# Kernel optimization log

Hardware: AMD Instinct MI355X
Metric: run time of the kernel (lower is better)

## Reference

```python
import jax, jax.numpy as jnp
import numpy as np

IMPOSSIBLE = -10000.0
K = 5  # BIOUL tag states per label: O, I, B, L, U


def _bioul_transitions():
    O, I, B, L, U = 0, 1, 2, 3, 4
    allowed = np.zeros((K, K), dtype=bool)
    for f, ts in {O: [O, B, U], B: [I, L], I: [I, L], L: [O, B, U], U: [O, B, U]}.items():
        allowed[f, ts] = True
    trans = jnp.asarray(np.where(allowed, 0.0, IMPOSSIBLE), dtype=jnp.float32)
    start = jnp.asarray([0.0, IMPOSSIBLE, 0.0, IMPOSSIBLE, 0.0], dtype=jnp.float32)  # O,B,U may start
    end = jnp.asarray([0.0, IMPOSSIBLE, IMPOSSIBLE, 0.0, 0.0], dtype=jnp.float32)    # O,L,U may end
    return trans, start, end


def _crf_marginal(emissions, mask):
    # Linear-chain CRF forward-backward log-marginals.
    # emissions: [N, T, K] float, mask: [N, T] bool (contiguous right-padded).
    trans, start, end = _bioul_transitions()
    e = jnp.swapaxes(emissions, 0, 1)   # [T, N, K]
    m = jnp.swapaxes(mask, 0, 1)        # [T, N]
    N = e.shape[1]

    alpha0 = start[None, :] + e[0]

    def fwd_step(alpha, xs):
        et, mt = xs
        new = jax.nn.logsumexp(alpha[:, :, None] + trans[None, :, :], axis=1) + et
        alpha = jnp.where(mt[:, None], new, alpha)  # carry alpha through padding
        return alpha, alpha

    alpha_last, alphas_rest = jax.lax.scan(fwd_step, alpha0, (e[1:], m[1:]))
    alphas = jnp.concatenate([alpha0[None], alphas_rest], axis=0)  # [T, N, K]
    logZ = jax.nn.logsumexp(alpha_last + end[None, :], axis=-1)    # [N]

    # Backward pass: beta_t excludes emission at t; beta at last valid token = end.
    m_next = jnp.concatenate([m[1:], jnp.zeros((1, N), dtype=bool)], axis=0)
    e_next = jnp.concatenate([e[1:], jnp.zeros_like(e[:1])], axis=0)

    def bwd_step(beta, xs):
        en, mt, mn = xs  # emis_{t+1}, mask_t, mask_{t+1}
        cand = jax.nn.logsumexp(trans[None, :, :] + (en + beta)[:, None, :], axis=2)
        beta = jnp.where((mt & ~mn)[:, None], end[None, :], cand)
        return beta, beta

    _, betas_rev = jax.lax.scan(
        bwd_step,
        jnp.broadcast_to(end, (N, K)),
        (e_next[::-1], m[::-1], m_next[::-1]),
    )
    betas = betas_rev[::-1]  # [T, N, K]

    logm = alphas + betas - logZ[None, :, None]
    return jnp.swapaxes(logm, 0, 1)  # [N, T, K]


def _forward(embeds, W, b, mask, tags):
    N, T, D = embeds.shape
    n_labels = tags.shape[1]
    logits = jnp.einsum('ntd,kd->ntk', embeds, W) + b  # [N, T, n_labels*K]
    crf_logits = logits.reshape(N, T, n_labels, K).transpose(0, 2, 1, 3).reshape(N * n_labels, T, K)
    crf_mask = jnp.repeat(mask, n_labels, axis=0)       # [N*n_labels, T] (repeat_interleave on dim 0)
    target = (tags[..., None] == jnp.arange(K)).reshape(N * n_labels, T, K)  # bool one-hot
    logm = _crf_marginal(crf_logits, crf_mask)
    lse = jax.nn.logsumexp(
        jnp.where(target, jax.nn.log_softmax(logm, axis=-1), IMPOSSIBLE), axis=-1
    )
    loss = -jnp.where(crf_mask, lse, 0.0).sum()
    return loss / 100.0


def setup_inputs() -> dict:
    key = jax.random.key(0)
    kE, kW, kb, kT, kL = jax.random.split(key, 5)
    N, T, D, n_labels = 64, 1024, 512, 24
    embeds = jax.random.normal(kE, (N, T, D), dtype=jnp.float32)
    W = jax.random.normal(kW, (n_labels * K, D), dtype=jnp.float32) * 0.02
    b = jax.random.normal(kb, (n_labels * K,), dtype=jnp.float32) * 0.02
    tags = jax.random.randint(kT, (N, n_labels, T), 0, K, dtype=jnp.int32)
    lengths = jax.random.randint(kL, (N,), T // 2, T + 1)
    mask = jnp.arange(T)[None, :] < lengths[:, None]  # right-padded variable lengths
    return {"embeds": embeds, "W": W, "b": b, "mask": mask, "tags": tags}


def reference(embeds, W, b, mask, tags):
    return _forward(embeds, W, b, mask, tags)
```

## Files before the change

### kernel.cpp

```cpp
#include <hip/hip_runtime.h>
#include <hip/hip_bf16.h>

#define IMP -10000.0f

#define O_BH   0u
#define O_BL   131072u
#define O_LEN  262144u
#define O_ACC  262400u
#define O_TT   262656u
#define O_E    6554112u
#define O_P    38011392u
#define O_Q    41157120u
#define O_FS   44302848u
#define O_BS   45875712u

typedef __attribute__((ext_vector_type(8))) short bf16x8;
typedef __attribute__((ext_vector_type(4))) float f32x4;

__device__ __forceinline__ float lse2(float a, float b) {
    float m = fmaxf(a, b);
    return m + __logf(__expf(a - m) + __expf(b - m));
}

__device__ __forceinline__ unsigned short f2bf(float x) {
    unsigned u = __float_as_uint(x);
    return (unsigned short)((u + 0x7FFFu + ((u >> 16) & 1u)) >> 16);
}
__device__ __forceinline__ float bf2f(unsigned short h) {
    return __uint_as_float(((unsigned)h) << 16);
}

__global__ __launch_bounds__(256) void prep_kernel(const unsigned char* __restrict__ mask,
                                                   int* __restrict__ lens,
                                                   double* __restrict__ acc) {
    int n = blockIdx.x;
    int tid = threadIdx.x;
    bool i32 = (mask[1] == 0);
    int cnt = 0;
    if (i32) {
        const int* m = (const int*)mask;
        for (int t = tid; t < 1024; t += 256) cnt += (m[n * 1024 + t] != 0);
    } else {
        for (int t = tid; t < 1024; t += 256) cnt += (mask[n * 1024 + t] != 0);
    }
    __shared__ int red[256];
    red[tid] = cnt;
    __syncthreads();
    for (int s = 128; s > 0; s >>= 1) {
        if (tid < s) red[tid] += red[tid + s];
        __syncthreads();
    }
    if (tid == 0) {
        lens[n] = red[0];
        if (n == 0) *acc = 0.0;
    }
}

__global__ __launch_bounds__(256) void tagsT_kernel(const int* __restrict__ tags,
                                                    int* __restrict__ tagsT) {
    int idx = blockIdx.x * 256 + threadIdx.x;
    int t = idx / 1536, s = idx - t * 1536;
    tagsT[idx] = tags[(size_t)s * 1024 + t];
}

__global__ __launch_bounds__(256) void prepW_kernel(const float* __restrict__ W,
                                                    short* __restrict__ Bh,
                                                    short* __restrict__ Bl) {
    int idx = blockIdx.x * 256 + threadIdx.x;
    int col = idx >> 9, k = idx & 511;
    float v = (col < 120) ? W[col * 512 + k] : 0.f;
    unsigned short h = f2bf(v);
    unsigned short l = f2bf(v - bf2f(h));
    int ct = col >> 4, c = col & 15;
    int kt = k >> 5, kg = (k >> 3) & 3, i = k & 7;
    size_t flat = ((size_t)(kt * 8 + ct) * 64 + kg * 16 + c) * 8 + i;
    Bh[flat] = (short)h;
    Bl[flat] = (short)l;
}

__global__ __launch_bounds__(256) void mfma_gemm(const float* __restrict__ A,
                                                 const short* __restrict__ Bh,
                                                 const short* __restrict__ Bl,
                                                 const float* __restrict__ bias,
                                                 float* __restrict__ E) {
    __shared__ short Ah[4][128][8];
    __shared__ short Al[4][128][8];
    int tid = threadIdx.x;
    int wave = tid >> 6, lane = tid & 63;
    long r0 = (long)blockIdx.x * 128;

    f32x4 acc[8][2];
#pragma unroll
    for (int rt = 0; rt < 8; ++rt)
#pragma unroll
        for (int ci = 0; ci < 2; ++ci) {
            acc[rt][ci][0] = 0.f; acc[rt][ci][1] = 0.f;
            acc[rt][ci][2] = 0.f; acc[rt][ci][3] = 0.f;
        }

    float bb[2];
#pragma unroll
    for (int ci = 0; ci < 2; ++ci) {
        int col = wave * 32 + ci * 16 + (lane & 15);
        bb[ci] = (col < 120) ? bias[col] : 0.f;
    }

    int arow = lane & 15;
    int akg = lane >> 4;

    for (int kt = 0; kt < 16; ++kt) {
        __syncthreads();
#pragma unroll
        for (int i = 0; i < 4; ++i) {
            int f = tid + (i << 8);
            int row = f >> 3, fq = f & 7;
            const float4 v = *(const float4*)(A + (r0 + row) * 512 + kt * 32 + fq * 4);
            int kgw = fq >> 1, i0 = (fq & 1) * 4;
            unsigned short h0 = f2bf(v.x), h1 = f2bf(v.y), h2 = f2bf(v.z), h3 = f2bf(v.w);
            short4 hv = make_short4((short)h0, (short)h1, (short)h2, (short)h3);
            short4 lv = make_short4((short)f2bf(v.x - bf2f(h0)), (short)f2bf(v.y - bf2f(h1)),
                                    (short)f2bf(v.z - bf2f(h2)), (short)f2bf(v.w - bf2f(h3)));
            *(short4*)&Ah[kgw][row][i0] = hv;
            *(short4*)&Al[kgw][row][i0] = lv;
        }
        __syncthreads();

        bf16x8 bh[2], bl[2];
#pragma unroll
        for (int ci = 0; ci < 2; ++ci) {
            int ct = wave * 2 + ci;
            size_t base = ((size_t)(kt * 8 + ct) * 64 + lane) * 8;
            bh[ci] = *(const bf16x8*)(Bh + base);
            bl[ci] = *(const bf16x8*)(Bl + base);
        }

#pragma unroll
        for (int rt = 0; rt < 8; ++rt) {
            bf16x8 ah = *(const bf16x8*)&Ah[akg][rt * 16 + arow][0];
            bf16x8 al = *(const bf16x8*)&Al[akg][rt * 16 + arow][0];
#pragma unroll
            for (int ci = 0; ci < 2; ++ci) {
                acc[rt][ci] = __builtin_amdgcn_mfma_f32_16x16x32_bf16(ah, bh[ci], acc[rt][ci], 0, 0, 0);
                acc[rt][ci] = __builtin_amdgcn_mfma_f32_16x16x32_bf16(ah, bl[ci], acc[rt][ci], 0, 0, 0);
                acc[rt][ci] = __builtin_amdgcn_mfma_f32_16x16x32_bf16(al, bh[ci], acc[rt][ci], 0, 0, 0);
            }
        }
    }

#pragma unroll
    for (int rt = 0; rt < 8; ++rt) {
#pragma unroll
        for (int ci = 0; ci < 2; ++ci) {
            int col = wave * 32 + ci * 16 + (lane & 15);
            if (col < 120) {
#pragma unroll
                for (int j = 0; j < 4; ++j) {
                    long r = r0 + rt * 16 + (lane >> 4) * 4 + j;
                    int n = (int)(r >> 10), t = (int)(r & 1023);
                    E[(size_t)t * 7680 + n * 120 + col] = acc[rt][ci][j] + bb[ci];
                }
            }
        }
    }
}

__global__ __launch_bounds__(256) void chunkops_kernel(const float* __restrict__ E,
                                                       const int* __restrict__ lens,
                                                       float* __restrict__ P,
                                                       float* __restrict__ Q,
                                                       float* __restrict__ BS) {
    int s = blockIdx.x * 256 + threadIdx.x;
    int c = blockIdx.y;
    int t0 = c << 3;
    int len = lens[s / 24];
    const float* ep = E + (size_t)t0 * 7680 + s * 5;
    bool fullQ = (t0 + 8 <= len - 1);

    float e[9][5];
#pragma unroll
    for (int j = 0; j < 8; ++j) {
        const float* q = ep + (size_t)j * 7680;
        e[j][0] = q[0]; e[j][1] = q[1]; e[j][2] = q[2]; e[j][3] = q[3]; e[j][4] = q[4];
    }
    if (fullQ) {
        const float* q = ep + (size_t)8 * 7680;
        e[8][0] = q[0]; e[8][1] = q[1]; e[8][2] = q[2]; e[8][3] = q[3]; e[8][4] = q[4];
    }

    {
        float r00 = lse2(e[0][0], e[0][4]), r01 = e[0][3], r10 = e[0][2], r11 = e[0][1];
#pragma unroll
        for (int j = 1; j < 8; ++j) {
            float m00 = lse2(e[j][0], e[j][4]), m01 = e[j][3], m10 = e[j][2], m11 = e[j][1];
            float n00 = lse2(m00 + r00, m01 + r10);
            float n01 = lse2(m00 + r01, m01 + r11);
            float n10 = lse2(m10 + r00, m11 + r10);
            float n11 = lse2(m10 + r01, m11 + r11);
            r00 = n00; r01 = n01; r10 = n10; r11 = n11;
        }
        float4 v; v.x = r00; v.y = r01; v.z = r10; v.w = r11;
        *(float4*)(P + ((size_t)c * 1536 + s) * 4) = v;
    }

    if (fullQ) {
        float r00 = lse2(e[1][0], e[1][4]), r01 = e[1][2], r10 = e[1][3], r11 = e[1][1];
#pragma unroll
        for (int j = 1; j < 8; ++j) {
            float g0 = e[j + 1][0], g1 = e[j + 1][1], g2 = e[j + 1][2], g3 = e[j + 1][3],
                  g4 = e[j + 1][4];
            float n00 = lse2(g0, g4), n01 = g2, n10 = g3, n11 = g1;
            float m00 = lse2(r00 + n00, r01 + n10);
            float m01 = lse2(r00 + n01, r01 + n11);
            float m10 = lse2(r10 + n00, r11 + n10);
            float m11 = lse2(r10 + n01, r11 + n11);
            r00 = m00; r01 = m01; r10 = m10; r11 = m11;
        }
        float4 v; v.x = r00; v.y = r01; v.z = r10; v.w = r11;
        *(float4*)(Q + ((size_t)c * 1536 + s) * 4) = v;
    } else if (t0 <= len - 1) {
        float X = 0.f, Y = IMP;
#pragma unroll
        for (int j = 6; j >= 0; --j) {
            if (t0 + j <= len - 2) {
                float g0 = e[j + 1][0], g1 = e[j + 1][1], g2 = e[j + 1][2], g3 = e[j + 1][3],
                      g4 = e[j + 1][4];
                float nX = lse2(lse2(g0, g4) + X, g2 + Y);
                float nY = lse2(g3 + X, g1 + Y);
                X = nX; Y = nY;
            }
        }
        float2 v; v.x = X; v.y = Y;
        *(float2*)(BS + ((size_t)c * 1536 + s) * 2) = v;
    }
}

__global__ __launch_bounds__(64) void combine_kernel(const float* __restrict__ P,
                                                     const float* __restrict__ Q,
                                                     const int* __restrict__ lens,
                                                     float* __restrict__ FS,
                                                     float* __restrict__ BS) {
    int s = blockIdx.x * 64 + threadIdx.x;
    float x = 0.f, y = IMP;
    for (int c = 0; c < 128; ++c) {
        float2 v; v.x = x; v.y = y;
        *(float2*)(FS + ((size_t)c * 1536 + s) * 2) = v;
        float4 p = *(const float4*)(P + ((size_t)c * 1536 + s) * 4);
        float nx = lse2(p.x + x, p.y + y);
        float ny = lse2(p.z + x, p.w + y);
        x = nx; y = ny;
    }
    int len = lens[s / 24];
    int cb = (len - 1) >> 3;
    float2 b = *(const float2*)(BS + ((size_t)cb * 1536 + s) * 2);
    float X = b.x, Y = b.y;
    for (int c = cb - 1; c >= 0; --c) {
        float4 q = *(const float4*)(Q + ((size_t)c * 1536 + s) * 4);
        float nX = lse2(q.x + X, q.y + Y);
        float nY = lse2(q.z + X, q.w + Y);
        X = nX; Y = nY;
        float2 v; v.x = X; v.y = Y;
        *(float2*)(BS + ((size_t)c * 1536 + s) * 2) = v;
    }
}

__global__ __launch_bounds__(256) void loss_kernel(const float* __restrict__ E,
                                                   const int* __restrict__ lens,
                                                   const float* __restrict__ FS,
                                                   const float* __restrict__ BS,
                                                   const int* __restrict__ tagsT,
                                                   double* __restrict__ acc) {
    int s = blockIdx.x * 256 + threadIdx.x;
    int c = blockIdx.y;
    int t0 = c << 3;
    int len = lens[s / 24];
    double Lv = 0.0;

    if (t0 < len) {
        int cb = (len - 1) >> 3;
        int nt = min(8, len - t0);
        const float* ep = E + (size_t)t0 * 7680 + s * 5;

        float ev[8][5];
#pragma unroll
        for (int j = 0; j < 8; ++j) {
            if (j < nt) {
                const float* q = ep + (size_t)j * 7680;
                ev[j][0] = q[0]; ev[j][1] = q[1]; ev[j][2] = q[2]; ev[j][3] = q[3]; ev[j][4] = q[4];
            }
        }
        float e8[5] = {0.f, 0.f, 0.f, 0.f, 0.f};
        if (c < cb) {
            const float* q = ep + (size_t)8 * 7680;
            e8[0] = q[0]; e8[1] = q[1]; e8[2] = q[2]; e8[3] = q[3]; e8[4] = q[4];
        }
        int tg[8];
#pragma unroll
        for (int j = 0; j < 8; ++j) tg[j] = tagsT[(size_t)(t0 + j) * 1536 + s];

        float2 f = *(const float2*)(FS + ((size_t)c * 1536 + s) * 2);
        float x = f.x, y = f.y;
        float xs[8], ys[8];
#pragma unroll
        for (int j = 0; j < 8; ++j) {
            if (j < nt) {
                xs[j] = x; ys[j] = y;
                float nx = lse2(lse2(ev[j][0], ev[j][4]) + x, ev[j][3] + y);
                float ny = lse2(ev[j][2] + x, ev[j][1] + y);
                x = nx; y = ny;
            }
        }

        float X = 0.f, Y = IMP;
        if (c < cb) {
            float2 bb = *(const float2*)(BS + ((size_t)(c + 1) * 1536 + s) * 2);
            X = bb.x; Y = bb.y;
        }
#pragma unroll
        for (int j = 7; j >= 0; --j) {
            if (j >= nt) continue;
            if (c == cb && j == nt - 1) {
                X = 0.f; Y = IMP;
            } else {
                float g0, g1, g2, g3, g4;
                if (j == 7) { g0 = e8[0]; g1 = e8[1]; g2 = e8[2]; g3 = e8[3]; g4 = e8[4]; }
                else { g0 = ev[j + 1][0]; g1 = ev[j + 1][1]; g2 = ev[j + 1][2];
                       g3 = ev[j + 1][3]; g4 = ev[j + 1][4]; }
                float nX = lse2(lse2(g0, g4) + X, g2 + Y);
                float nY = lse2(g3 + X, g1 + Y);
                X = nX; Y = nY;
            }
            float v0 = xs[j] + ev[j][0] + X, v1 = ys[j] + ev[j][1] + Y, v2 = xs[j] + ev[j][2] + Y;
            float v3 = ys[j] + ev[j][3] + X, v4 = xs[j] + ev[j][4] + X;
            int tag = tg[j];
            float m = fmaxf(fmaxf(fmaxf(fmaxf(v0, v1), v2), v3), v4);
            float ssum = __expf(v0 - m) + __expf(v1 - m) + __expf(v2 - m) +
                         __expf(v3 - m) + __expf(v4 - m);
            float lse = m + __logf(ssum);
            float vt = (tag == 0) ? v0 : (tag == 1) ? v1 : (tag == 2) ? v2 : (tag == 3) ? v3 : v4;
            float ls = vt - lse;
            float mm = fmaxf(ls, IMP);
            float term = mm + __logf(__expf(ls - mm) + 4.0f * __expf(IMP - mm));
            Lv += (double)term;
        }
    }

    __shared__ double red[256];
    red[threadIdx.x] = Lv;
    __syncthreads();
    for (int st = 128; st > 0; st >>= 1) {
        if (threadIdx.x < st) red[threadIdx.x] += red[threadIdx.x + st];
        __syncthreads();
    }
    if (threadIdx.x == 0) atomicAdd(acc, red[0]);
}

__global__ void finalize_kernel(const double* __restrict__ acc, float* __restrict__ out) {
    out[0] = (float)(-(*acc) * 0.01);
}

extern "C" void kernel_launch(void* const* d_in, const int* in_sizes, int n_in,
                              void* d_out, int out_size, void* d_ws, size_t ws_size,
                              hipStream_t stream) {
    const float* embeds = (const float*)d_in[0];
    const float* W = (const float*)d_in[1];
    const float* bias = (const float*)d_in[2];
    const unsigned char* mask = (const unsigned char*)d_in[3];
    const int* tags = (const int*)d_in[4];
    float* out = (float*)d_out;

    char* ws = (char*)d_ws;
    short* Bh = (short*)(ws + O_BH);
    short* Bl = (short*)(ws + O_BL);
    int* lens = (int*)(ws + O_LEN);
    double* acc = (double*)(ws + O_ACC);
    int* tagsT = (int*)(ws + O_TT);
    float* E = (float*)(ws + O_E);
    float* P = (float*)(ws + O_P);
    float* Q = (float*)(ws + O_Q);
    float* FS = (float*)(ws + O_FS);
    float* BS = (float*)(ws + O_BS);

    prep_kernel<<<64, 256, 0, stream>>>(mask, lens, acc);
    prepW_kernel<<<256, 256, 0, stream>>>(W, Bh, Bl);
    tagsT_kernel<<<6144, 256, 0, stream>>>(tags, tagsT);
    mfma_gemm<<<512, 256, 0, stream>>>(embeds, Bh, Bl, bias, E);
    chunkops_kernel<<<dim3(6, 128), 256, 0, stream>>>(E, lens, P, Q, BS);
    combine_kernel<<<24, 64, 0, stream>>>(P, Q, lens, FS, BS);
    loss_kernel<<<dim3(6, 128), 256, 0, stream>>>(E, lens, FS, BS, tagsT, acc);
    finalize_kernel<<<1, 1, 0, stream>>>(acc, out);
}
```

Before: 329.9 us.

## Replace serial chunk combine with parallel log-semiring prefix scan

New measurement: 273.8 us. 17.0% less time.

```diff
diff --git a/kernel.cpp b/kernel.cpp
--- a/kernel.cpp
+++ b/kernel.cpp
@@ -20,6 +20,15 @@
 __device__ __forceinline__ float lse2(float a, float b) {
     float m = fmaxf(a, b);
     return m + __logf(__expf(a - m) + __expf(b - m));
+}
+
+__device__ __forceinline__ float4 matmul22(float4 A, float4 B) {
+    float4 r;
+    r.x = lse2(A.x + B.x, A.y + B.z);
+    r.y = lse2(A.x + B.y, A.y + B.w);
+    r.z = lse2(A.z + B.x, A.w + B.z);
+    r.w = lse2(A.z + B.y, A.w + B.w);
+    return r;
 }
 
 __device__ __forceinline__ unsigned short f2bf(float x) {
@@ -234,32 +243,64 @@
     }
 }
 
-__global__ __launch_bounds__(64) void combine_kernel(const float* __restrict__ P,
-                                                     const float* __restrict__ Q,
-                                                     const int* __restrict__ lens,
-                                                     float* __restrict__ FS,
-                                                     float* __restrict__ BS) {
-    int s = blockIdx.x * 64 + threadIdx.x;
-    float x = 0.f, y = IMP;
-    for (int c = 0; c < 128; ++c) {
-        float2 v; v.x = x; v.y = y;
-        *(float2*)(FS + ((size_t)c * 1536 + s) * 2) = v;
-        float4 p = *(const float4*)(P + ((size_t)c * 1536 + s) * 4);
-        float nx = lse2(p.x + x, p.y + y);
-        float ny = lse2(p.z + x, p.w + y);
-        x = nx; y = ny;
-    }
+__global__ __launch_bounds__(128) void combine_kernel(const float* __restrict__ P,
+                                                      const float* __restrict__ Q,
+                                                      const int* __restrict__ lens,
+                                                      float* __restrict__ FS,
+                                                      float* __restrict__ BS) {
+    int s = blockIdx.x;
+    int c = threadIdx.x;
+    __shared__ float4 ops[128];
+
+    float4 v = *(const float4*)(P + ((size_t)c * 1536 + s) * 4);
+    ops[c] = v;
+    __syncthreads();
+#pragma unroll
+    for (int d = 1; d < 128; d <<= 1) {
+        float4 other;
+        bool act = (c >= d);
+        if (act) other = ops[c - d];
+        __syncthreads();
+        if (act) { v = matmul22(v, other); ops[c] = v; }
+        __syncthreads();
+    }
+    float2 fs;
+    if (c == 0) {
+        fs.x = 0.f; fs.y = IMP;
+    } else {
+        float4 m = ops[c - 1];
+        fs.x = lse2(m.x, m.y + IMP);
+        fs.y = lse2(m.z, m.w + IMP);
+    }
+    *(float2*)(FS + ((size_t)c * 1536 + s) * 2) = fs;
+
     int len = lens[s / 24];
     int cb = (len - 1) >> 3;
     float2 b = *(const float2*)(BS + ((size_t)cb * 1536 + s) * 2);
-    float X = b.x, Y = b.y;
-    for (int c = cb - 1; c >= 0; --c) {
-        float4 q = *(const float4*)(Q + ((size_t)c * 1536 + s) * 4);
-        float nX = lse2(q.x + X, q.y + Y);
-        float nY = lse2(q.z + X, q.w + Y);
-        X = nX; Y = nY;
-        float2 v; v.x = X; v.y = Y;
-        *(float2*)(BS + ((size_t)c * 1536 + s) * 2) = v;
+    __syncthreads();
+
+    float4 r;
+    if (c < cb) {
+        r = *(const float4*)(Q + ((size_t)c * 1536 + s) * 4);
+    } else {
+        r.x = 0.f; r.y = IMP; r.z = IMP; r.w = 0.f;
+    }
+    ops[c] = r;
+    __syncthreads();
+#pragma unroll
+    for (int d = 1; d < 128; d <<= 1) {
+        float4 other;
+        bool act = (c + d) < 128;
+        if (act) other = ops[c + d];
+        __syncthreads();
+        if (act) { r = matmul22(r, other); ops[c] = r; }
+        __syncthreads();
+    }
+    if (c < cb) {
+        float2 bs;
+        bs.x = lse2(r.x + b.x, r.y + b.y);
+        bs.y = lse2(r.z + b.x, r.w + b.y);
+        *(float2*)(BS + ((size_t)c * 1536 + s) * 2) = bs;
     }
 }
 
@@ -385,7 +426,7 @@
     tagsT_kernel<<<6144, 256, 0, stream>>>(tags, tagsT);
     mfma_gemm<<<512, 256, 0, stream>>>(embeds, Bh, Bl, bias, E);
     chunkops_kernel<<<dim3(6, 128), 256, 0, stream>>>(E, lens, P, Q, BS);
-    combine_kernel<<<24, 64, 0, stream>>>(P, Q, lens, FS, BS);
+    combine_kernel<<<1536, 128, 0, stream>>>(P, Q, lens, FS, BS);
     loss_kernel<<<dim3(6, 128), 256, 0, stream>>>(E, lens, FS, BS, tagsT, acc);
     finalize_kernel<<<1, 1, 0, stream>>>(acc, out);
 }
```
